# Optimization experiments

Hardware: AMD Instinct MI355X
Metric: run time of the kernel (lower is better)

## Reference

```python
import jax, jax.numpy as jnp
import numpy as np

G = 64      # norm_groups
T = 5       # Newton-Schulz iterations
EPS = 1e-5


def setup_inputs() -> dict:
    key = jax.random.key(0)
    weight = jax.random.normal(key, (2048, 18432), dtype=jnp.float32)
    return {"weight": weight}


def reference(weight):
    out_ch = weight.shape[0]
    # Z: [G, c, d] with c = out_ch // G, d = prod(rest)
    Z = weight.reshape(G, out_ch // G, -1)
    Zc = Z - jnp.mean(Z, axis=-1, keepdims=True)
    # S = Zc @ Zc^T : [G, c, c]
    S = jnp.einsum('gcd,ged->gce', Zc, Zc)
    c = S.shape[-1]
    eye = jnp.eye(c, dtype=S.dtype)
    S = S + EPS * eye
    # Frobenius norm per group, keepdim -> [G,1,1]
    norm_S = jnp.sqrt(jnp.sum(S * S, axis=(1, 2), keepdims=True))
    S = S / norm_S
    # Newton-Schulz: B_{t+1} = 1.5*B_t - 0.5 * B_t^3 @ S
    B = jnp.broadcast_to(eye, S.shape)
    for _ in range(T):
        B3 = jnp.matmul(jnp.matmul(B, B), B)
        B = 1.5 * B - 0.5 * jnp.matmul(B3, S)
    W = jnp.matmul(B, Zc) / jnp.sqrt(norm_S)
    return W.reshape(weight.shape)
```

## Files before the change

### kernel.cpp

```cpp
#include <hip/hip_runtime.h>

#define G 64
#define C 32
#define D 18432
#define NCH 16
#define TD (D / NCH)
#define NST (TD / 128)
#define EPS 1e-5f
#define NS_ITERS 5

typedef __attribute__((ext_vector_type(8))) short short8v;
typedef __attribute__((ext_vector_type(4))) float float4v;

__device__ __forceinline__ void split3(float x, unsigned short& h1,
                                       unsigned short& h2, unsigned short& h3) {
    unsigned int u = __float_as_uint(x);
    unsigned int m1 = u & 0xffff0000u;
    float r1 = x - __uint_as_float(m1);
    unsigned int u2 = __float_as_uint(r1);
    unsigned int m2 = u2 & 0xffff0000u;
    float r2 = r1 - __uint_as_float(m2);
    h1 = (unsigned short)(m1 >> 16);
    h2 = (unsigned short)(m2 >> 16);
    h3 = (unsigned short)(__float_as_uint(r2) >> 16);
}

__device__ __forceinline__ void split8(const float4& v0, const float4& v1,
                                       short8v& p1, short8v& p2, short8v& p3,
                                       float& rs) {
    float x[8] = {v0.x, v0.y, v0.z, v0.w, v1.x, v1.y, v1.z, v1.w};
#pragma unroll
    for (int j = 0; j < 8; ++j) {
        unsigned short h1, h2, h3;
        rs += x[j];
        split3(x[j], h1, h2, h3);
        p1[j] = (short)h1; p2[j] = (short)h2; p3[j] = (short)h3;
    }
}

#define MM6(T, A0, A1, A2, B0, B1, B2)                                        \
    T = __builtin_amdgcn_mfma_f32_16x16x32_bf16(A0, B0, T, 0, 0, 0);          \
    T = __builtin_amdgcn_mfma_f32_16x16x32_bf16(A0, B1, T, 0, 0, 0);          \
    T = __builtin_amdgcn_mfma_f32_16x16x32_bf16(A1, B0, T, 0, 0, 0);          \
    T = __builtin_amdgcn_mfma_f32_16x16x32_bf16(A1, B1, T, 0, 0, 0);          \
    T = __builtin_amdgcn_mfma_f32_16x16x32_bf16(A0, B2, T, 0, 0, 0);          \
    T = __builtin_amdgcn_mfma_f32_16x16x32_bf16(A2, B0, T, 0, 0, 0);

__global__ __launch_bounds__(256) void k1_gram(const float* __restrict__ W,
                                               float* __restrict__ psum,
                                               float* __restrict__ prow) {
    __shared__ float red[4 * 1056 + 4 * C];

    const int ch   = blockIdx.x;
    const int g    = blockIdx.y;
    const int bid  = g * NCH + ch;
    const int tid  = threadIdx.x;
    const int lane = tid & 63;
    const int wave = tid >> 6;

    const int rbase = lane & 15;
    const int koff  = (lane >> 4) * 8;

    const float* Zg = W + (size_t)g * C * D + (size_t)ch * TD;
    const float* p0 = Zg + (size_t)rbase * D + wave * 32 + koff;
    const float* p1 = p0 + (size_t)16 * D;

    float4v acc00 = (float4v)0.f, acc01 = (float4v)0.f;
    float4v acc10 = (float4v)0.f, acc11 = (float4v)0.f;
    float rs0 = 0.f, rs1 = 0.f;

    float4 c00 = *(const float4*)(p0);
    float4 c01 = *(const float4*)(p0 + 4);
    float4 c10 = *(const float4*)(p1);
    float4 c11 = *(const float4*)(p1 + 4);

#pragma unroll 1
    for (int st = 0; st < NST; ++st) {
        float4 n00, n01, n10, n11;
        if (st + 1 < NST) {
            const float* q0 = p0 + (st + 1) * 128;
            const float* q1 = p1 + (st + 1) * 128;
            n00 = *(const float4*)(q0);
            n01 = *(const float4*)(q0 + 4);
            n10 = *(const float4*)(q1);
            n11 = *(const float4*)(q1 + 4);
        }
        short8v fa0, fa1, fa2, fb0, fb1, fb2;
        split8(c00, c01, fa0, fa1, fa2, rs0);
        split8(c10, c11, fb0, fb1, fb2, rs1);

        MM6(acc00, fa0, fa1, fa2, fa0, fa1, fa2)
        MM6(acc01, fa0, fa1, fa2, fb0, fb1, fb2)
        MM6(acc10, fb0, fb1, fb2, fa0, fa1, fa2)
        MM6(acc11, fb0, fb1, fb2, fb0, fb1, fb2)

        c00 = n00; c01 = n01; c10 = n10; c11 = n11;
    }

    rs0 += __shfl_xor(rs0, 16, 64); rs0 += __shfl_xor(rs0, 32, 64);
    rs1 += __shfl_xor(rs1, 16, 64); rs1 += __shfl_xor(rs1, 32, 64);
    if (lane < 16) {
        red[4224 + wave * C + lane]      = rs0;
        red[4224 + wave * C + 16 + lane] = rs1;
    }

    {
        const int rq  = (lane >> 4) << 2;
        const int cl  = lane & 15;
        float* base = red + wave * 1056;
#pragma unroll
        for (int j = 0; j < 4; ++j) {
            base[(rq + j) * 33 + cl]            = acc00[j];
            base[(rq + j) * 33 + 16 + cl]       = acc01[j];
            base[(16 + rq + j) * 33 + cl]       = acc10[j];
            base[(16 + rq + j) * 33 + 16 + cl]  = acc11[j];
        }
    }
    __syncthreads();

#pragma unroll
    for (int k = 0; k < 4; ++k) {
        int el = tid + 256 * k;
        int row = el >> 5, col = el & 31;
        int o = row * 33 + col;
        float sv = red[o] + red[1056 + o] + red[2112 + o] + red[3168 + o];
        psum[(size_t)bid * (C * C) + el] = sv;
    }
    if (tid < C) {
        float s = red[4224 + tid] + red[4224 + C + tid] +
                  red[4224 + 2 * C + tid] + red[4224 + 3 * C + tid];
        prow[(size_t)bid * C + tid] = s;
    }
}

__global__ __launch_bounds__(256) void k2_ns(const float* __restrict__ psum,
                                             const float* __restrict__ prow,
                                             float* __restrict__ MT,
                                             float* __restrict__ vout) {
    __shared__ float S[C][C + 1];
    __shared__ float B[C][C + 1];
    __shared__ float T1[C][C + 1];
    __shared__ float T2[C][C + 1];
    __shared__ float mean[C];
    __shared__ float redw[4];
    __shared__ float normsh;

    const int g   = blockIdx.x;
    const int tid = threadIdx.x;
    const int e   = tid & 31;
    const int cbq = tid >> 5;

    float selt[4];
#pragma unroll
    for (int k = 0; k < 4; ++k) {
        int el = tid + 256 * k;
        float s = 0.f;
#pragma unroll
        for (int ch = 0; ch < NCH; ++ch)
            s += psum[((size_t)g * NCH + ch) * (C * C) + el];
        selt[k] = s;
    }
    if (tid < C) {
        float s = 0.f;
#pragma unroll
        for (int ch = 0; ch < NCH; ++ch)
            s += prow[((size_t)g * NCH + ch) * C + tid];
        mean[tid] = s / (float)D;
    }
    __syncthreads();

    float ss = 0.f;
#pragma unroll
    for (int k = 0; k < 4; ++k) {
        int el = tid + 256 * k;
        int c = el >> 5;
        float sv = selt[k] - (float)D * mean[c] * mean[e];
        if (c == e) sv += EPS;
        S[c][e] = sv;
        ss = fmaf(sv, sv, ss);
    }
#pragma unroll
    for (int off = 32; off >= 1; off >>= 1) ss += __shfl_xor(ss, off, 64);
    if ((tid & 63) == 0) redw[tid >> 6] = ss;
    __syncthreads();
    if (tid == 0) normsh = sqrtf(redw[0] + redw[1] + redw[2] + redw[3]);
    __syncthreads();
    const float inv_norm = 1.0f / normsh;
#pragma unroll
    for (int k = 0; k < 4; ++k) {
        int c = cbq + 8 * k;
        S[c][e] *= inv_norm;
        B[c][e] = (c == e) ? 1.f : 0.f;
    }
    __syncthreads();

    for (int it = 0; it < NS_ITERS; ++it) {
#pragma unroll
        for (int k = 0; k < 4; ++k) {
            int c = cbq + 8 * k;
            float s = 0.f;
            for (int kk = 0; kk < C; ++kk)
                s = fmaf(B[c][kk], B[kk][e], s);
            T1[c][e] = s;
        }
        __syncthreads();
#pragma unroll
        for (int k = 0; k < 4; ++k) {
            int c = cbq + 8 * k;
            float s = 0.f;
            for (int kk = 0; kk < C; ++kk)
                s = fmaf(T1[c][kk], B[kk][e], s);
            T2[c][e] = s;
        }
        __syncthreads();
        float pv[4];
#pragma unroll
        for (int k = 0; k < 4; ++k) {
            int c = cbq + 8 * k;
            float s = 0.f;
            for (int kk = 0; kk < C; ++kk)
                s = fmaf(T2[c][kk], S[kk][e], s);
            pv[k] = s;
        }
#pragma unroll
        for (int k = 0; k < 4; ++k) {
            int c = cbq + 8 * k;
            B[c][e] = 1.5f * B[c][e] - 0.5f * pv[k];
        }
        __syncthreads();
    }

    const float invs = 1.0f / sqrtf(normsh);
#pragma unroll
    for (int k = 0; k < 4; ++k) {
        int c = cbq + 8 * k;
        MT[(size_t)g * (C * C) + e * C + c] = B[c][e] * invs;
    }
    if (tid < C) {
        float s = 0.f;
        for (int ee = 0; ee < C; ++ee)
            s = fmaf(B[tid][ee] * invs, mean[ee], s);
        vout[(size_t)g * C + tid] = s;
    }
}

__global__ __launch_bounds__(256) void k3_apply(const float* __restrict__ W,
                                                const float* __restrict__ MT,
                                                const float* __restrict__ vv,
                                                float* __restrict__ out) {
    const int blocksPerGroup = D / 512;
    const int g   = blockIdx.x / blocksPerGroup;
    const int cbk = blockIdx.x % blocksPerGroup;
    const int d0  = cbk * 512 + (int)threadIdx.x * 2;
    const float* Zg = W + (size_t)g * C * D + d0;
    const float* Mg = MT + (size_t)g * (C * C);

    float accx[C], accy[C];
#pragma unroll
    for (int r = 0; r < C; ++r) { accx[r] = 0.f; accy[r] = 0.f; }

    for (int e = 0; e < C; ++e) {
        float2 z = *(const float2*)(Zg + (size_t)e * D);
#pragma unroll
        for (int r = 0; r < C; ++r) {
            float m = Mg[e * C + r];
            accx[r] = fmaf(m, z.x, accx[r]);
            accy[r] = fmaf(m, z.y, accy[r]);
        }
    }

    float* Og = out + (size_t)g * C * D + d0;
#pragma unroll
    for (int r = 0; r < C; ++r) {
        float vr = vv[g * C + r];
        float2 o = make_float2(accx[r] - vr, accy[r] - vr);
        *(float2*)(Og + (size_t)r * D) = o;
    }
}

extern "C" void kernel_launch(void* const* d_in, const int* in_sizes, int n_in,
                              void* d_out, int out_size, void* d_ws, size_t ws_size,
                              hipStream_t stream) {
    const float* w = (const float*)d_in[0];
    float* out = (float*)d_out;

    float* psum = (float*)d_ws;
    float* prow = psum + (size_t)(G * NCH) * (C * C);
    float* MT   = prow + (size_t)(G * NCH) * C;
    float* vv   = MT   + (size_t)G * (C * C);

    k1_gram<<<dim3(NCH, G), 256, 0, stream>>>(w, psum, prow);
    k2_ns  <<<G,            256, 0, stream>>>(psum, prow, MT, vv);
    k3_apply<<<G * (D / 512), 256, 0, stream>>>(w, MT, vv, out);
}
```

Before: 95.80 us.

## Stage Gram kernel input through double-buffered LDS with async global-to-LDS loads

The Gram kernel now copies each 32x256 tile of the weight into shared memory with global_load_lds, double-buffered, and waits on vmcnt before a barrier. Previously each wave loaded its fragments straight from global memory with a one-step register prefetch. The chunk count per group is halved, so there are fewer blocks and partial sums, and each block runs a longer loop. The change adds two barriers per step and LDS traffic, and fewer blocks may reduce occupancy across the CUs.

```diff
diff --git a/kernel.cpp b/kernel.cpp
--- a/kernel.cpp
+++ b/kernel.cpp
@@ -3,14 +3,17 @@
 #define G 64
 #define C 32
 #define D 18432
-#define NCH 16
+#define NCH 8
 #define TD (D / NCH)
-#define NST (TD / 128)
+#define SUB 256
+#define NST (TD / SUB)
 #define EPS 1e-5f
 #define NS_ITERS 5
 
 typedef __attribute__((ext_vector_type(8))) short short8v;
 typedef __attribute__((ext_vector_type(4))) float float4v;
+typedef __attribute__((address_space(1))) const void g_void;
+typedef __attribute__((address_space(3))) void l_void;
 
 __device__ __forceinline__ void split3(float x, unsigned short& h1,
                                        unsigned short& h2, unsigned short& h3) {
@@ -46,10 +49,22 @@
     T = __builtin_amdgcn_mfma_f32_16x16x32_bf16(A0, B2, T, 0, 0, 0);          \
     T = __builtin_amdgcn_mfma_f32_16x16x32_bf16(A2, B0, T, 0, 0, 0);
 
+#define STAGE(BUF, ST)                                                         \
+    {                                                                          \
+        _Pragma("unroll")                                                      \
+        for (int i_ = 0; i_ < 8; ++i_) {                                       \
+            const int r_ = wave * 8 + i_;                                      \
+            const float* src_ = Zg + (size_t)r_ * D + (ST) * SUB + lane * 4;   \
+            __builtin_amdgcn_global_load_lds((g_void*)src_,                    \
+                                             (l_void*)&lds[BUF][r_][0],        \
+                                             16, 0, 0);                        \
+        }                                                                      \
+    }
+
 __global__ __launch_bounds__(256) void k1_gram(const float* __restrict__ W,
                                                float* __restrict__ psum,
                                                float* __restrict__ prow) {
-    __shared__ float red[4 * 1056 + 4 * C];
+    __shared__ __align__(16) float lds[2][32][SUB];
 
     const int ch   = blockIdx.x;
     const int g    = blockIdx.y;
@@ -58,62 +73,67 @@
     const int lane = tid & 63;
     const int wave = tid >> 6;
 
-    const int rbase = lane & 15;
-    const int koff  = (lane >> 4) * 8;
-
     const float* Zg = W + (size_t)g * C * D + (size_t)ch * TD;
-    const float* p0 = Zg + (size_t)rbase * D + wave * 32 + koff;
-    const float* p1 = p0 + (size_t)16 * D;
+
+    const int rA   = lane & 15;
+    const int rB   = 16 + rA;
+    const int koff = (lane >> 4) << 3;
 
     float4v acc00 = (float4v)0.f, acc01 = (float4v)0.f;
     float4v acc10 = (float4v)0.f, acc11 = (float4v)0.f;
     float rs0 = 0.f, rs1 = 0.f;
 
-    float4 c00 = *(const float4*)(p0);
-    float4 c01 = *(const float4*)(p0 + 4);
-    float4 c10 = *(const float4*)(p1);
-    float4 c11 = *(const float4*)(p1 + 4);
-
-#pragma unroll 1
+    STAGE(0, 0);
+
     for (int st = 0; st < NST; ++st) {
-        float4 n00, n01, n10, n11;
+        const int buf = st & 1;
+        asm volatile("" ::: "memory");
+        __builtin_amdgcn_s_barrier();
+        asm volatile("" ::: "memory");
         if (st + 1 < NST) {
-            const float* q0 = p0 + (st + 1) * 128;
-            const float* q1 = p1 + (st + 1) * 128;
-            n00 = *(const float4*)(q0);
-            n01 = *(const float4*)(q0 + 4);
-            n10 = *(const float4*)(q1);
-            n11 = *(const float4*)(q1 + 4);
-        }
-        short8v fa0, fa1, fa2, fb0, fb1, fb2;
-        split8(c00, c01, fa0, fa1, fa2, rs0);
-        split8(c10, c11, fb0, fb1, fb2, rs1);
-
-        MM6(acc00, fa0, fa1, fa2, fa0, fa1, fa2)
-        MM6(acc01, fa0, fa1, fa2, fb0, fb1, fb2)
-        MM6(acc10, fb0, fb1, fb2, fa0, fa1, fa2)
-        MM6(acc11, fb0, fb1, fb2, fb0, fb1, fb2)
-
-        c00 = n00; c01 = n01; c10 = n10; c11 = n11;
+            STAGE(buf ^ 1, st + 1);
+            asm volatile("s_waitcnt vmcnt(8)" ::: "memory");
+        } else {
+            asm volatile("s_waitcnt vmcnt(0)" ::: "memory");
+        }
+        __builtin_amdgcn_s_barrier();
+        asm volatile("" ::: "memory");
+
+#pragma unroll
+        for (int ks = 0; ks < 2; ++ks) {
+            const int colf = (wave << 6) + (ks << 5) + koff;
+            float4 a0 = *(const float4*)&lds[buf][rA][colf];
+            float4 a1 = *(const float4*)&lds[buf][rA][colf + 4];
+            float4 b0 = *(const float4*)&lds[buf][rB][colf];
+            float4 b1 = *(const float4*)&lds[buf][rB][colf + 4];
+            short8v fa0, fa1, fa2, fb0, fb1, fb2;
+            split8(a0, a1, fa0, fa1, fa2, rs0);
+            split8(b0, b1, fb0, fb1, fb2, rs1);
+            MM6(acc00, fa0, fa1, fa2, fa0, fa1, fa2)
+            MM6(acc01, fa0, fa1, fa2, fb0, fb1, fb2)
+            MM6(acc10, fb0, fb1, fb2, fa0, fa1, fa2)
+            MM6(acc11, fb0, fb1, fb2, fb0, fb1, fb2)
+        }
     }
 
     rs0 += __shfl_xor(rs0, 16, 64); rs0 += __shfl_xor(rs0, 32, 64);
     rs1 += __shfl_xor(rs1, 16, 64); rs1 += __shfl_xor(rs1, 32, 64);
+
+    __syncthreads();
+    float* red = (float*)lds;
     if (lane < 16) {
         red[4224 + wave * C + lane]      = rs0;
         red[4224 + wave * C + 16 + lane] = rs1;
     }
-
     {
-        const int rq  = (lane >> 4) << 2;
-        const int cl  = lane & 15;
+        const int rq = (lane >> 4) << 2;
         float* base = red + wave * 1056;
 #pragma unroll
         for (int j = 0; j < 4; ++j) {
-            base[(rq + j) * 33 + cl]            = acc00[j];
-            base[(rq + j) * 33 + 16 + cl]       = acc01[j];
-            base[(16 + rq + j) * 33 + cl]       = acc10[j];
-            base[(16 + rq + j) * 33 + 16 + cl]  = acc11[j];
+            base[(rq + j) * 33 + rA]           = acc00[j];
+            base[(rq + j) * 33 + 16 + rA]      = acc01[j];
+            base[(16 + rq + j) * 33 + rA]      = acc10[j];
+            base[(16 + rq + j) * 33 + 16 + rA] = acc11[j];
         }
     }
     __syncthreads();
```

Result: slower. 99.07 us (+3.4%).
